# Kernel tuning notes

Hardware: AMD Instinct MI355X
Metric: run time of the kernel (lower is better)

The kernel has to match this reference:

```python
import jax, jax.numpy as jnp
import numpy as np

LAGRANGE_ORDER = 5  # fixed, as in the torch module


def _lagrange_weights(alpha):
    """Vectorised Lagrange weights of length L+1. alpha: [B,N] -> [B,N,L+1]."""
    L = LAGRANGE_ORDER
    j = jnp.arange(L + 1, dtype=alpha.dtype)
    u = alpha[..., None] - j                          # [B,N,L+1]
    denom = j[:, None] - j[None, :]                   # [L+1,L+1]
    mask = ~jnp.eye(L + 1, dtype=bool)
    num = jnp.where(mask, u[..., None, :], jnp.ones_like(u)[..., None, :])
    den = jnp.where(mask, denom, jnp.ones_like(denom))
    return (num / den).prod(axis=-1)                  # [B,N,L+1]


def setup_inputs() -> dict:
    key = jax.random.key(0)
    k1, k2, k3 = jax.random.split(key, 3)
    B, N = 16, 16384
    # fractional period in samples, in [40, 100) -> max floor(f0)=99, K=99+5+3=107<=108
    f0 = 40.0 + 60.0 * jax.random.uniform(k1, (B, N), dtype=jnp.float32)
    x = jax.random.normal(k2, (B, N), dtype=jnp.float32)
    l_b = jax.random.uniform(k3, (B, N, 2), dtype=jnp.float32)  # (g, p) in [0,1]
    return {"f0": f0, "x": x, "l_b": l_b, "K": 108}


def reference(f0, x, l_b, K):
    B, N = x.shape
    L = LAGRANGE_ORDER
    # design_loop: (g, p) -> loop taps [b0, a1]; gain capped <1 for stability
    g = 0.99 * l_b[..., 0]
    p = l_b[..., 1]
    b0 = g * (1.0 - p)                                # [B,N]
    a1 = g * p
    # tune_f0: subtract low-frequency phase delay of (b0 + a1 z^-1)
    f0c = f0 - a1 / (b0 + a1 + 1e-7)
    # Lagrange centre & weights
    z = jnp.floor(f0c).astype(jnp.int32)
    z_center = z - L // 2                             # [B,N]
    alpha = f0c - z_center.astype(f0.dtype)
    w = _lagrange_weights(alpha)                      # [B,N,L+1]
    # compute_resonator_matrix: loop filter convolved with fractional delay -> block [B,N,L+2]
    block = (b0[..., None] * jnp.pad(w, ((0, 0), (0, 0), (0, 1)))
             + a1[..., None] * jnp.pad(w, ((0, 0), (0, 0), (1, 0))))
    # scatter (-block) into A; LPC lag k+1 lives in column k
    cols = z_center[..., None] - 1 + jnp.arange(L + 2)  # [B,N,L+2]
    cols = jnp.clip(cols, 0, K - 1)
    A = jnp.zeros((B, N, K), x.dtype).at[
        jnp.arange(B)[:, None, None], jnp.arange(N)[None, :, None], cols
    ].add(-block)
    # sample_wise_lpc: y[n] = x[n] - sum_k A[n,k] * y[n-1-k], zero init state
    def step(buf, inp):
        a_n, x_n = inp                                 # [B,K], [B]
        y_n = x_n - jnp.sum(a_n * buf, axis=-1)
        buf = jnp.concatenate([y_n[:, None], buf[:, :-1]], axis=1)
        return buf, y_n
    buf0 = jnp.zeros((B, K), x.dtype)
    _, ys = jax.lax.scan(step, buf0, (A.transpose(1, 0, 2), x.T))  # ys: [N,B]
    return ys.T
```

## Files before the change

kernel.cpp:

```cpp
#include <hip/hip_runtime.h>
#include <math.h>


#define B_    16
#define N_    16384
#define S_    16
#define NSEG  1024
#define NITER 28
#define RUNS  104
#define CHUNK 37

#define TG_FLOATS (B_ * S_ * RUNS * RUNS)

__device__ __forceinline__ void diffks_coeffs(float f0v, float lbg, float lbp,
                                              int n, float4& lo, float4& hi) {
  float g  = 0.99f * lbg;
  float p  = lbp;
  float b0 = g * (1.0f - p);
  float a1 = g * p;
  float f0c = f0v - a1 / (b0 + a1 + 1e-7f);
  int   zc  = (int)floorf(f0c) - 2;
  float alpha = f0c - (float)zc;
  float u0 = alpha;
  float u1 = alpha - 1.0f;
  float u2 = alpha - 2.0f;
  float u3 = alpha - 3.0f;
  float u4 = alpha - 4.0f;
  float u5 = alpha - 5.0f;
  float w0 = u1 * u2 * u3 * u4 * u5 * (-1.0f / 120.0f);
  float w1 = u0 * u2 * u3 * u4 * u5 * ( 1.0f /  24.0f);
  float w2 = u0 * u1 * u3 * u4 * u5 * (-1.0f /  12.0f);
  float w3 = u0 * u1 * u2 * u4 * u5 * ( 1.0f /  12.0f);
  float w4 = u0 * u1 * u2 * u3 * u5 * (-1.0f /  24.0f);
  float w5 = u0 * u1 * u2 * u3 * u4 * ( 1.0f / 120.0f);
  lo.x = b0 * w0;
  lo.y = fmaf(b0, w1, a1 * w0);
  lo.z = fmaf(b0, w2, a1 * w1);
  lo.w = fmaf(b0, w3, a1 * w2);
  hi.x = fmaf(b0, w4, a1 * w3);
  hi.y = fmaf(b0, w5, a1 * w4);
  hi.z = a1 * w5;
  hi.w = __int_as_float((n - 6 - zc) & 255);
}

__global__ __launch_bounds__(1024) void diffks_phase1(
    const float* __restrict__ f0, const float* __restrict__ lb,
    const float* __restrict__ x, float* __restrict__ Tg) {
  const int bs = blockIdx.x;
  const int b  = bs >> 4, s = bs & 15;
  const int n0 = s << 10;
  const int tid = threadIdx.x;

  __shared__ __align__(16) float hist[256 * RUNS];
  __shared__ float4 sLo[NSEG], sHi[NSEG];
  __shared__ float  sX[NSEG];

  {
    const size_t gi = (size_t)b * N_ + n0 + tid;
    float4 lo, hi;
    diffks_coeffs(f0[gi], lb[2 * gi], lb[2 * gi + 1], tid, lo, hi);
    sLo[tid] = lo; sHi[tid] = hi; sX[tid] = x[gi];
  }
  for (int i = tid; i < 64 * RUNS; i += 1024)
    ((float4*)hist)[i] = float4{0.0f, 0.0f, 0.0f, 0.0f};
  __syncthreads();
  if (tid < 103) hist[(255 - tid) * RUNS + tid] = 1.0f;
  __syncthreads();

  const int w    = tid >> 6;
  const int lane = tid & 63;
  const int cl   = 2 * lane;
  const bool act = (lane < 52);
  const bool px  = (lane == 51);

  for (int t = 0; t < 32; ++t) {
#pragma unroll
    for (int u = 0; u < 2; ++u) {
      const int p = 32 * t + 2 * w + u;
      const float4 lo = sLo[p];
      const float4 hi = sHi[p];
      const float  xv = sX[p];
      if (act) {
        const int base = __float_as_int(hi.w);
        float2 acc;
        acc.x = 0.0f;
        acc.y = px ? xv : 0.0f;
        const float c[7] = {hi.z, hi.y, hi.x, lo.w, lo.z, lo.y, lo.x};
#pragma unroll
        for (int m = 0; m < 7; ++m) {
          const int row = (base + m) & 255;
          const float2 v = *(const float2*)&hist[row * RUNS + cl];
          acc.x = fmaf(c[m], v.x, acc.x);
          acc.y = fmaf(c[m], v.y, acc.y);
        }
        *(float2*)&hist[(p & 255) * RUNS + cl] = acc;
      }
    }
    __syncthreads();
  }

  float* __restrict__ T = Tg + (size_t)bs * RUNS * RUNS;
  for (int idx = tid; idx < RUNS * RUNS; idx += 1024) {
    const int r = idx / RUNS;
    const int j = idx - r * RUNS;
    T[idx] = (j < 103) ? hist[((255 - j) & 255) * RUNS + r] : 0.0f;
  }
}


#define CG_LOAD(BUF, Tbase, rbase)                                           \
  { _Pragma("unroll") for (int kk = 0; kk < 13; ++kk)                        \
      BUF[kk] = *(const float2*)&(Tbase)[((rbase) + kk) * RUNS + cl]; }

#define CG_FMA(BUF, rbase)                                                   \
  { _Pragma("unroll") for (int kk = 0; kk < 13; ++kk) {                      \
      const float cv = curL[(rbase) + kk];                                   \
      acc[kk & 3].x = fmaf(BUF[kk].x, cv, acc[kk & 3].x);                    \
      acc[kk & 3].y = fmaf(BUF[kk].y, cv, acc[kk & 3].y); } }

__global__ __launch_bounds__(256, 1) void diffks_compose_scan(
    const float* __restrict__ Tg, const float* __restrict__ f0,
    const float* __restrict__ lb, const float* __restrict__ x,
    float* __restrict__ y) {
  const int bs = blockIdx.x;
  const int b  = bs >> 4, s = bs & 15;
  const int n0 = s << 10;
  const int tid = threadIdx.x;

  __shared__ __align__(16) float ring[512];
  __shared__ __align__(16) float4 sC[2 * NSEG];
  __shared__ float  sX[NSEG];
  __shared__ float  sY[NSEG];
  __shared__ float  curL[RUNS];

  ring[tid] = 0.0f; ring[tid + 256] = 0.0f;
  if (tid < 52) {
    float2 iv; iv.x = 0.0f; iv.y = (tid == 51) ? 1.0f : 0.0f;
    *(float2*)&curL[2 * tid] = iv;
  }
  __syncthreads();

  if (tid < 64) {
    const int l  = tid;
    const int cl = 2 * l;
    if (l < 52 && s > 0) {
      const float* __restrict__ Tb = Tg + (size_t)(b * S_) * RUNS * RUNS;
      float2 B0[13], B1[13], B2[13], B3[13];
      float2 acc[4];
      CG_LOAD(B0, Tb, 0)
      CG_LOAD(B1, Tb, 13)
      CG_LOAD(B2, Tb, 26)
      CG_LOAD(B3, Tb, 39)
      for (int k = 0; k < s; ++k) {
        const float* __restrict__ Tk = Tb + (size_t)k * RUNS * RUNS;
        const float* __restrict__ Tn =
            Tb + (size_t)((k + 1 < s) ? k + 1 : k) * RUNS * RUNS;
#pragma unroll
        for (int a = 0; a < 4; ++a) { acc[a].x = 0.0f; acc[a].y = 0.0f; }
        CG_FMA(B0, 0)   CG_LOAD(B0, Tk, 52)
        CG_FMA(B1, 13)  CG_LOAD(B1, Tk, 65)
        CG_FMA(B2, 26)  CG_LOAD(B2, Tk, 78)
        CG_FMA(B3, 39)  CG_LOAD(B3, Tk, 91)
        CG_FMA(B0, 52)  CG_LOAD(B0, Tn, 0)
        CG_FMA(B1, 65)  CG_LOAD(B1, Tn, 13)
        CG_FMA(B2, 78)  CG_LOAD(B2, Tn, 26)
        CG_FMA(B3, 91)  CG_LOAD(B3, Tn, 39)
        float2 nw;
        nw.x = (acc[0].x + acc[1].x) + (acc[2].x + acc[3].x);
        nw.y = (acc[0].y + acc[1].y) + (acc[2].y + acc[3].y);
        if (l == 51) nw.y = 1.0f;
        *(float2*)&curL[cl] = nw;
        __builtin_amdgcn_wave_barrier();
        asm volatile("" ::: "memory");
      }
    }
    __builtin_amdgcn_wave_barrier();
    asm volatile("" ::: "memory");
    {
      const float v = curL[l];
      ring[255 - l] = v; ring[511 - l] = v;
      if (l < 39) {
        const float v2 = curL[l + 64];
        ring[191 - l] = v2; ring[447 - l] = v2;
      }
    }
  } else {
    const size_t gb = (size_t)b * N_ + n0;
    for (int i = tid - 64; i < NSEG; i += 192) {
      const size_t gi = gb + i;
      float4 lo, hi;
      diffks_coeffs(f0[gi], lb[2 * gi], lb[2 * gi + 1], n0 + i, lo, hi);
      sC[2 * i] = lo; sC[2 * i + 1] = hi; sX[i] = x[gi];
    }
  }
  __syncthreads();

  if (tid < 64) {
    const int lane = tid;
    const bool act = (lane < CHUNK);
    for (int t = 0; t < NITER; ++t) {
      const int p = t * CHUNK + lane;
      if (act && p < NSEG) {
        const float4 lo = sC[2 * p];
        const float4 hi = sC[2 * p + 1];
        const float  xv = sX[p];
        const int base = __float_as_int(hi.w);
        const float r0 = ring[base + 0];
        const float r1 = ring[base + 1];
        const float r2 = ring[base + 2];
        const float r3 = ring[base + 3];
        const float r4 = ring[base + 4];
        const float r5 = ring[base + 5];
        const float r6 = ring[base + 6];
        const float s0 = fmaf(lo.x, r6, xv);
        const float s1 = fmaf(lo.y, r5, lo.z * r4);
        const float s2 = fmaf(lo.w, r3, hi.x * r2);
        const float s3 = fmaf(hi.y, r1, hi.z * r0);
        const float yv = (s0 + s1) + (s2 + s3);
        const int wsl = p & 255;
        ring[wsl]       = yv;
        ring[wsl + 256] = yv;
        sY[p] = yv;
      }
      __builtin_amdgcn_wave_barrier();
      asm volatile("" ::: "memory");
    }
  }
  __syncthreads();

  float4* __restrict__ yb = (float4*)(y + (size_t)b * N_ + n0);
  yb[tid] = ((const float4*)sY)[tid];
}

__global__ __launch_bounds__(256) void diffks_coeff_fb(
    const float* __restrict__ f0, const float* __restrict__ lb,
    float* __restrict__ cw, int total, int Nmask) {
  int idx = blockIdx.x * blockDim.x + threadIdx.x;
  if (idx >= total) return;
  float4 lo, hi;
  diffks_coeffs(f0[idx], lb[2 * idx], lb[2 * idx + 1], idx & Nmask, lo, hi);
  float4* out4 = (float4*)cw;
  out4[2 * idx]     = lo;
  out4[2 * idx + 1] = hi;
}

__global__ __launch_bounds__(64) void diffks_scan_fb(
    const float* __restrict__ x, const float* __restrict__ cw,
    float* __restrict__ y, int N) {
  const int b    = blockIdx.x;
  const int lane = threadIdx.x;
  __shared__ float ring[512];
#pragma unroll
  for (int i = 0; i < 8; ++i) ring[lane + 64 * i] = 0.0f;
  __builtin_amdgcn_wave_barrier();
  asm volatile("" ::: "memory");
  const float4* __restrict__ c4 = (const float4*)(cw + (size_t)b * N * 8);
  const float*  __restrict__ xb = x + (size_t)b * N;
  float*        __restrict__ yb = y + (size_t)b * N;
  const bool act = (lane < CHUNK);
  const int nIter = (N + CHUNK - 1) / CHUNK;
  for (int t = 0; t < nIter; ++t) {
    const int n = t * CHUNK + lane;
    if (act && n < N) {
      const float4 lo = c4[2 * n];
      const float4 hi = c4[2 * n + 1];
      const float  xv = xb[n];
      const int base = __float_as_int(hi.w);
      const float r0 = ring[base + 0];
      const float r1 = ring[base + 1];
      const float r2 = ring[base + 2];
      const float r3 = ring[base + 3];
      const float r4 = ring[base + 4];
      const float r5 = ring[base + 5];
      const float r6 = ring[base + 6];
      const float s0 = fmaf(lo.x, r6, xv);
      const float s1 = fmaf(lo.y, r5, lo.z * r4);
      const float s2 = fmaf(lo.w, r3, hi.x * r2);
      const float s3 = fmaf(hi.y, r1, hi.z * r0);
      const float yv = (s0 + s1) + (s2 + s3);
      ring[n & 255]         = yv;
      ring[(n & 255) + 256] = yv;
      yb[n] = yv;
    }
    __builtin_amdgcn_wave_barrier();
    asm volatile("" ::: "memory");
  }
}

extern "C" void kernel_launch(void* const* d_in, const int* in_sizes, int n_in,
                              void* d_out, int out_size, void* d_ws, size_t ws_size,
                              hipStream_t stream) {
  const float* f0 = (const float*)d_in[0];
  const float* x  = (const float*)d_in[1];
  const float* lb = (const float*)d_in[2];
  float* out = (float*)d_out;

  const int total = in_sizes[0];
  const size_t need = (size_t)TG_FLOATS * 4;

  if (total == B_ * N_ && ws_size >= need) {
    float* Tg = (float*)d_ws;
    diffks_phase1<<<B_ * S_, 1024, 0, stream>>>(f0, lb, x, Tg);
    diffks_compose_scan<<<B_ * S_, 256, 0, stream>>>(Tg, f0, lb, x, out);
  } else {
    const int N = total / B_;
    float* cw = (float*)d_ws;
    diffks_coeff_fb<<<(total + 255) / 256, 256, 0, stream>>>(f0, lb, cw, total, N - 1);
    diffks_scan_fb<<<B_, 64, 0, stream>>>(x, cw, out, N);
  }
}
```

Before: 112.9 us.

## Split segment-state composition into a separate kernel computed once per batch

Segment initial states were recomposed redundantly in every scan block (block s did s matrix-vector steps). A new small kernel chains the transition matrices once per batch row and stores all segment states to workspace, and the scan kernel just loads its state. Input loads in the scan kernel are also batched/vectorized. This removes quadratic redundant work but adds an extra launch and serializes the compose chain before the scan rather than overlapping it with coefficient setup.

```diff
diff --git a/kernel.cpp b/kernel.cpp
--- a/kernel.cpp
+++ b/kernel.cpp
@@ -11,6 +11,7 @@
 #define CHUNK 37
 
 #define TG_FLOATS (B_ * S_ * RUNS * RUNS)
+#define ST_FLOATS (B_ * S_ * RUNS)
 
 __device__ __forceinline__ void diffks_coeffs(float f0v, float lbg, float lbp,
                                               int n, float4& lo, float4& hi) {
@@ -118,9 +119,60 @@
       acc[kk & 3].x = fmaf(BUF[kk].x, cv, acc[kk & 3].x);                    \
       acc[kk & 3].y = fmaf(BUF[kk].y, cv, acc[kk & 3].y); } }
 
-__global__ __launch_bounds__(256, 1) void diffks_compose_scan(
-    const float* __restrict__ Tg, const float* __restrict__ f0,
-    const float* __restrict__ lb, const float* __restrict__ x,
+__global__ __launch_bounds__(64) void diffks_compose(
+    const float* __restrict__ Tg, float* __restrict__ states) {
+  const int b = blockIdx.x;
+  const int l = threadIdx.x;
+  const int cl = 2 * l;
+  __shared__ float curL[RUNS];
+
+  float* __restrict__ stb = states + (size_t)b * S_ * RUNS;
+  if (l < 52) {
+    float2 iv; iv.x = 0.0f; iv.y = (l == 51) ? 1.0f : 0.0f;
+    *(float2*)&curL[cl] = iv;
+    float2 z;  z.x = 0.0f;  z.y = 0.0f;
+    *(float2*)&stb[cl] = z;
+  }
+  __builtin_amdgcn_wave_barrier();
+  asm volatile("" ::: "memory");
+
+  if (l < 52) {
+    const float* __restrict__ Tb = Tg + (size_t)(b * S_) * RUNS * RUNS;
+    float2 B0[13], B1[13], B2[13], B3[13];
+    float2 acc[4];
+    CG_LOAD(B0, Tb, 0)
+    CG_LOAD(B1, Tb, 13)
+    CG_LOAD(B2, Tb, 26)
+    CG_LOAD(B3, Tb, 39)
+    for (int k = 0; k < S_ - 1; ++k) {
+      const float* __restrict__ Tk = Tb + (size_t)k * RUNS * RUNS;
+      const float* __restrict__ Tn =
+          Tb + (size_t)((k + 1 < S_ - 1) ? k + 1 : k) * RUNS * RUNS;
+#pragma unroll
+      for (int a = 0; a < 4; ++a) { acc[a].x = 0.0f; acc[a].y = 0.0f; }
+      CG_FMA(B0, 0)   CG_LOAD(B0, Tk, 52)
+      CG_FMA(B1, 13)  CG_LOAD(B1, Tk, 65)
+      CG_FMA(B2, 26)  CG_LOAD(B2, Tk, 78)
+      CG_FMA(B3, 39)  CG_LOAD(B3, Tk, 91)
+      CG_FMA(B0, 52)  CG_LOAD(B0, Tn, 0)
+      CG_FMA(B1, 65)  CG_LOAD(B1, Tn, 13)
+      CG_FMA(B2, 78)  CG_LOAD(B2, Tn, 26)
+      CG_FMA(B3, 91)  CG_LOAD(B3, Tn, 39)
+      float2 nw;
+      nw.x = (acc[0].x + acc[1].x) + (acc[2].x + acc[3].x);
+      nw.y = (acc[0].y + acc[1].y) + (acc[2].y + acc[3].y);
+      if (l == 51) nw.y = 1.0f;
+      *(float2*)&curL[cl] = nw;
+      *(float2*)&stb[(k + 1) * RUNS + cl] = nw;
+      __builtin_amdgcn_wave_barrier();
+      asm volatile("" ::: "memory");
+    }
+  }
+}
+
+__global__ __launch_bounds__(256) void diffks_phase3(
+    const float* __restrict__ f0, const float* __restrict__ lb,
+    const float* __restrict__ x, const float* __restrict__ states,
     float* __restrict__ y) {
   const int bs = blockIdx.x;
   const int b  = bs >> 4, s = bs & 15;
@@ -128,70 +180,37 @@
   const int tid = threadIdx.x;
 
   __shared__ __align__(16) float ring[512];
-  __shared__ __align__(16) float4 sC[2 * NSEG];
+  __shared__ float4 sC[2 * NSEG];
   __shared__ float  sX[NSEG];
   __shared__ float  sY[NSEG];
-  __shared__ float  curL[RUNS];
-
-  ring[tid] = 0.0f; ring[tid + 256] = 0.0f;
-  if (tid < 52) {
-    float2 iv; iv.x = 0.0f; iv.y = (tid == 51) ? 1.0f : 0.0f;
-    *(float2*)&curL[2 * tid] = iv;
-  }
-  __syncthreads();
-
-  if (tid < 64) {
-    const int l  = tid;
-    const int cl = 2 * l;
-    if (l < 52 && s > 0) {
-      const float* __restrict__ Tb = Tg + (size_t)(b * S_) * RUNS * RUNS;
-      float2 B0[13], B1[13], B2[13], B3[13];
-      float2 acc[4];
-      CG_LOAD(B0, Tb, 0)
-      CG_LOAD(B1, Tb, 13)
-      CG_LOAD(B2, Tb, 26)
-      CG_LOAD(B3, Tb, 39)
-      for (int k = 0; k < s; ++k) {
-        const float* __restrict__ Tk = Tb + (size_t)k * RUNS * RUNS;
-        const float* __restrict__ Tn =
-            Tb + (size_t)((k + 1 < s) ? k + 1 : k) * RUNS * RUNS;
-#pragma unroll
-        for (int a = 0; a < 4; ++a) { acc[a].x = 0.0f; acc[a].y = 0.0f; }
-        CG_FMA(B0, 0)   CG_LOAD(B0, Tk, 52)
-        CG_FMA(B1, 13)  CG_LOAD(B1, Tk, 65)
-        CG_FMA(B2, 26)  CG_LOAD(B2, Tk, 78)
-        CG_FMA(B3, 39)  CG_LOAD(B3, Tk, 91)
-        CG_FMA(B0, 52)  CG_LOAD(B0, Tn, 0)
-        CG_FMA(B1, 65)  CG_LOAD(B1, Tn, 13)
-        CG_FMA(B2, 78)  CG_LOAD(B2, Tn, 26)
-        CG_FMA(B3, 91)  CG_LOAD(B3, Tn, 39)
-        float2 nw;
-        nw.x = (acc[0].x + acc[1].x) + (acc[2].x + acc[3].x);
-        nw.y = (acc[0].y + acc[1].y) + (acc[2].y + acc[3].y);
-        if (l == 51) nw.y = 1.0f;
-        *(float2*)&curL[cl] = nw;
-        __builtin_amdgcn_wave_barrier();
-        asm volatile("" ::: "memory");
-      }
-    }
-    __builtin_amdgcn_wave_barrier();
-    asm volatile("" ::: "memory");
-    {
-      const float v = curL[l];
-      ring[255 - l] = v; ring[511 - l] = v;
-      if (l < 39) {
-        const float v2 = curL[l + 64];
-        ring[191 - l] = v2; ring[447 - l] = v2;
-      }
-    }
-  } else {
+
+#pragma unroll
+  for (int k = 0; k < 2; ++k) ring[tid + 256 * k] = 0.0f;
+  {
     const size_t gb = (size_t)b * N_ + n0;
-    for (int i = tid - 64; i < NSEG; i += 192) {
-      const size_t gi = gb + i;
+    const float*  __restrict__ f0b = f0 + gb;
+    const float2* __restrict__ lbb = (const float2*)(lb + 2 * gb);
+    const float*  __restrict__ xb  = x + gb;
+    float  vf[4]; float2 vl[4]; float vx[4];
+#pragma unroll
+    for (int k = 0; k < 4; ++k) {
+      const int i = tid + 256 * k;
+      vf[k] = f0b[i]; vl[k] = lbb[i]; vx[k] = xb[i];
+    }
+#pragma unroll
+    for (int k = 0; k < 4; ++k) {
+      const int i = tid + 256 * k;
       float4 lo, hi;
-      diffks_coeffs(f0[gi], lb[2 * gi], lb[2 * gi + 1], n0 + i, lo, hi);
-      sC[2 * i] = lo; sC[2 * i + 1] = hi; sX[i] = x[gi];
-    }
+      diffks_coeffs(vf[k], vl[k].x, vl[k].y, n0 + i, lo, hi);
+      sC[2 * i] = lo; sC[2 * i + 1] = hi; sX[i] = vx[k];
+    }
+  }
+  __syncthreads();
+  const float* __restrict__ st = states + (size_t)bs * RUNS;
+  if (tid < 103) {
+    const float v = st[tid];
+    ring[255 - tid] = v;
+    ring[511 - tid] = v;
   }
   __syncthreads();
 
@@ -296,12 +315,14 @@
   float* out = (float*)d_out;
 
   const int total = in_sizes[0];
-  const size_t need = (size_t)TG_FLOATS * 4;
+  const size_t need = (size_t)(TG_FLOATS + ST_FLOATS) * 4;
 
   if (total == B_ * N_ && ws_size >= need) {
     float* Tg = (float*)d_ws;
+    float* st = Tg + TG_FLOATS;
     diffks_phase1<<<B_ * S_, 1024, 0, stream>>>(f0, lb, x, Tg);
-    diffks_compose_scan<<<B_ * S_, 256, 0, stream>>>(Tg, f0, lb, x, out);
+    diffks_compose<<<B_, 64, 0, stream>>>(Tg, st);
+    diffks_phase3<<<B_ * S_, 256, 0, stream>>>(f0, lb, x, st, out);
   } else {
     const int N = total / B_;
     float* cw = (float*)d_ws;
```

Result: slower. 117.5 us (+4.1%).
